# Optimization experiments

Hardware: AMD Instinct MI355X
Metric: run time of the kernel (lower is better)

## Reference

```python
import jax, jax.numpy as jnp
import numpy as np

B, H, NCAND = 2048, 1024, 4  # batch, hidden_size, l candidates


def setup_inputs() -> dict:
    key = jax.random.key(0)
    ks = jax.random.split(key, 5)
    s = 1.0 / np.sqrt(H)  # torch uniform(-1/sqrt(H), 1/sqrt(H)) init
    L = jax.random.uniform(ks[0], (NCAND, H, H), minval=-s, maxval=s, dtype=jnp.float32)
    R = jax.random.uniform(ks[1], (NCAND, H, H), minval=-s, maxval=s, dtype=jnp.float32)
    # candidate 3 is initialized to identity in the original module
    L = L.at[3].set(jnp.eye(H, dtype=jnp.float32))
    R = R.at[3].set(jnp.eye(H, dtype=jnp.float32))
    b = jnp.zeros((NCAND, H), dtype=jnp.float32)
    w_score = jax.random.uniform(ks[2], (H,), minval=-s, maxval=s, dtype=jnp.float32)
    x = jax.random.normal(ks[3], (B, 1, H), dtype=jnp.float32)
    h_prev = jax.random.normal(ks[4], (B, 1, H), dtype=jnp.float32)
    return {"x": x, "h_prev": h_prev, "L": L, "R": R, "b": b, "w_score": w_score}


def _mix(lst, w_score):
    # lst: [B, 4, H] candidate vectors; score each candidate, softmax-combine.
    scores = jnp.einsum('bkh,h->bk', lst, w_score)          # [B, 4]
    probs = jax.nn.softmax(scores, axis=-1)
    out = jnp.einsum('bk,bkh->bh', probs, lst)              # [B, H]
    return out, jnp.argmax(scores, axis=-1)


def _lin(v, W):
    # v: [B, H], W: [4, H, H] -> all 4 candidate transforms: [B, 4, H]
    return jnp.einsum('bh,khd->bkd', v, W)


def reference(x, h_prev, L, R, b, w_score):
    xs = x[:, 0, :]        # [B, H]
    hs = h_prev[:, 0, :]   # [B, H]
    bb = b[None]           # [1, 4, H]

    z1 = jax.nn.sigmoid(xs @ L[0] + hs @ R[0] + b[0])
    r = jax.nn.sigmoid(xs @ L[1] + hs @ R[1] + b[1])
    z2 = jax.nn.sigmoid(xs @ L[0] + hs @ R[0] + b[0])  # identical expression to z1, as in source

    # stage 3: rh = mix_k( (h@Lk) * (r@Rk) + bk )
    rh, g3 = _mix(_lin(hs, L) * _lin(r, R) + bb, w_score)
    # stage 4: h_tilde = mix_k( tanh(x@Lk + rh@Rk + bk) )
    h_tilde, g4 = _mix(jnp.tanh(_lin(xs, L) + _lin(rh, R) + bb), w_score)
    # stage 5: 1 - (z1@Rk + bk)
    one_minus_z1, g5 = _mix(1.0 - (_lin(z1, R) + bb), w_score)
    # stage 6: (h_tilde@Lk) * (one_minus_z1@Rk) + bk
    zh_tilde, g6 = _mix(_lin(h_tilde, L) * _lin(one_minus_z1, R) + bb, w_score)
    # stage 7: (h@Lk) * (z2@Rk) + bk
    z2h, g7 = _mix(_lin(hs, L) * _lin(z2, R) + bb, w_score)
    # stage 8: zh_tilde@Lk + z2h@Rk + bk
    h_next, g8 = _mix(_lin(zh_tilde, L) + _lin(z2h, R) + bb, w_score)

    G = jnp.zeros((x.shape[0], 9), dtype=jnp.int32)
    G = (G.at[:, 3].set(g3).at[:, 4].set(g4).at[:, 5].set(g5)
          .at[:, 6].set(g6).at[:, 7].set(g7).at[:, 8].set(g8))
    return h_next[:, None, :], G
```

## Files before the change

### kernel.cpp

```cpp
#include <hip/hip_runtime.h>
#include <math.h>

#define B 2048
#define H 1024
#define HH (1024 * 1024)

typedef __attribute__((ext_vector_type(8))) short bf16x8;
typedef __attribute__((ext_vector_type(4))) float floatx4;

__device__ __forceinline__ short bf16_rne(float x) {
    unsigned int b = __float_as_uint(x);
    unsigned int r = (b + 0x7fffu + ((b >> 16) & 1u)) >> 16;
    return (short)r;
}
__device__ __forceinline__ float bf16_f(short h) {
    return __uint_as_float(((unsigned int)(unsigned short)h) << 16);
}
__device__ __forceinline__ void split2(float x, short& h, short& l) {
    h = bf16_rne(x);
    l = bf16_rne(x - bf16_f(h));
}
__device__ __forceinline__ float ld3(const float* f, const short* h, const short* l, size_t i) {
    if (f) return f[i];
    return bf16_f(h[i]) + bf16_f(l[i]);
}

__device__ __forceinline__ void gl16(const void* g, void* l) {
    __builtin_amdgcn_global_load_lds(
        (const __attribute__((address_space(1))) void*)g,
        (__attribute__((address_space(3))) void*)l, 16, 0, 0);
}

struct Job {
    const short* ah; const short* al;
    const short* wh; const short* wl;
    float* c;
    long ldc;
};
struct Jobs { Job j[8]; };

__global__ __launch_bounds__(256, 2) void gemm_kernel(Jobs jobs)
{
    __shared__ short lds[2][4][4096];
    const int bid = blockIdx.x;
    const int z = bid >> 7;
    const int mi = (bid & 127) >> 3, ni = bid & 7;
    const Job jb = jobs.j[z];
    const int tid = threadIdx.x;
    const int w = tid >> 6, lane = tid & 63;
    const int wm = w >> 1, wn = w & 1;
    const int m0 = mi * 128, n0 = ni * 128;

    const int cid0 = tid, cid1 = 256 + tid;
    const int r0 = cid0 >> 2, g0 = (((cid0 & 3) ^ ((cid0 >> 3) & 3)) << 3);
    const int r1 = cid1 >> 2, g1 = (((cid1 & 3) ^ ((cid1 >> 3) & 3)) << 3);

    const short* p0[4] = { jb.ah + (size_t)(m0 + r0) * H + g0,
                           jb.al + (size_t)(m0 + r0) * H + g0,
                           jb.wh + (size_t)(n0 + r0) * H + g0,
                           jb.wl + (size_t)(n0 + r0) * H + g0 };
    const short* p1[4] = { jb.ah + (size_t)(m0 + r1) * H + g1,
                           jb.al + (size_t)(m0 + r1) * H + g1,
                           jb.wh + (size_t)(n0 + r1) * H + g1,
                           jb.wl + (size_t)(n0 + r1) * H + g1 };

    const int fr = lane & 15, kc = lane >> 4;
    int aoff[4], boff[4];
#pragma unroll
    for (int t = 0; t < 4; t++) {
        int ar = wm * 64 + t * 16 + fr;
        aoff[t] = ar * 32 + ((kc ^ ((ar >> 1) & 3)) << 3);
        int br = wn * 64 + t * 16 + fr;
        boff[t] = br * 32 + ((kc ^ ((br >> 1) & 3)) << 3);
    }

    floatx4 acc[4][4];
#pragma unroll
    for (int i = 0; i < 4; i++)
#pragma unroll
        for (int j = 0; j < 4; j++) acc[i][j] = (floatx4)0.f;

#define ISSUE8(P)                                                        \
    do {                                                                 \
        _Pragma("unroll")                                                \
        for (int o = 0; o < 4; o++) {                                    \
            gl16(p0[o], &lds[P][o][w * 512]);                            \
            gl16(p1[o], &lds[P][o][2048 + w * 512]);                     \
            p0[o] += 32; p1[o] += 32;                                    \
        }                                                                \
    } while (0)

#define COMPUTE(P)                                                       \
    do {                                                                 \
        bf16x8 fah[4], fal[4], fbh[4], fbl[4];                           \
        _Pragma("unroll")                                                \
        for (int t = 0; t < 4; t++) {                                    \
            fah[t] = *(const bf16x8*)&lds[P][0][aoff[t]];                \
            fal[t] = *(const bf16x8*)&lds[P][1][aoff[t]];                \
            fbh[t] = *(const bf16x8*)&lds[P][2][boff[t]];                \
            fbl[t] = *(const bf16x8*)&lds[P][3][boff[t]];                \
        }                                                                \
        _Pragma("unroll")                                                \
        for (int mt = 0; mt < 4; mt++)                                   \
            _Pragma("unroll")                                            \
            for (int nt = 0; nt < 4; nt++) {                             \
                acc[mt][nt] = __builtin_amdgcn_mfma_f32_16x16x32_bf16(fah[mt], fbh[nt], acc[mt][nt], 0, 0, 0); \
                acc[mt][nt] = __builtin_amdgcn_mfma_f32_16x16x32_bf16(fah[mt], fbl[nt], acc[mt][nt], 0, 0, 0); \
                acc[mt][nt] = __builtin_amdgcn_mfma_f32_16x16x32_bf16(fal[mt], fbh[nt], acc[mt][nt], 0, 0, 0); \
                acc[mt][nt] = __builtin_amdgcn_mfma_f32_16x16x32_bf16(fal[mt], fbl[nt], acc[mt][nt], 0, 0, 0); \
            }                                                            \
    } while (0)

    ISSUE8(0);
    for (int ks = 0; ks < 32; ks += 2) {
        __syncthreads();
        ISSUE8(1);
        COMPUTE(0);
        __syncthreads();
        if (ks + 2 < 32) ISSUE8(0);
        COMPUTE(1);
    }
#undef ISSUE8
#undef COMPUTE

    const int cr = (lane >> 4) * 4, cc = lane & 15;
#pragma unroll
    for (int mt = 0; mt < 4; mt++)
#pragma unroll
        for (int nt = 0; nt < 4; nt++) {
            float* Cp = jb.c + (size_t)(m0 + wm * 64 + mt * 16 + cr) * jb.ldc
                             + n0 + wn * 64 + nt * 16 + cc;
#pragma unroll
            for (int i = 0; i < 4; i++) Cp[(size_t)i * jb.ldc] = acc[mt][nt][i];
        }
}

__global__ __launch_bounds__(256) void wsplit_kernel(
    const float* __restrict__ L, const float* __restrict__ R,
    short* __restrict__ Lth, short* __restrict__ Ltl,
    short* __restrict__ Rth, short* __restrict__ Rtl)
{
    const int zz = blockIdx.z;
    const float* W = (zz < 3) ? L : R;
    short* Oh = (zz < 3) ? Lth : Rth;
    short* Ol = (zz < 3) ? Ltl : Rtl;
    const int z = (zz < 3) ? zz : zz - 3;
    const int k0 = blockIdx.y * 32, n0 = blockIdx.x * 32;
    __shared__ float t[32][33];
    const int tx = threadIdx.x & 31, ty = threadIdx.x >> 5;
    const float* src = W + (size_t)z * HH;
#pragma unroll
    for (int j = 0; j < 4; j++) {
        int r = ty + j * 8;
        t[r][tx] = src[(size_t)(k0 + r) * 1024 + n0 + tx];
    }
    __syncthreads();
    short* oh = Oh + (size_t)z * HH;
    short* ol = Ol + (size_t)z * HH;
#pragma unroll
    for (int j = 0; j < 4; j++) {
        int n = ty + j * 8;
        float v = t[tx][n];
        short hh, ll; split2(v, hh, ll);
        oh[(size_t)(n0 + n) * 1024 + k0 + tx] = hh;
        ol[(size_t)(n0 + n) * 1024 + k0 + tx] = ll;
    }
}

__global__ __launch_bounds__(256) void conv_kernel(
    const float* __restrict__ xs, const float* __restrict__ hs,
    short* __restrict__ xh, short* __restrict__ xl,
    short* __restrict__ hh, short* __restrict__ hl)
{
    size_t i = (size_t)blockIdx.x * 256 + threadIdx.x;
    short a, b2; split2(xs[i], a, b2); xh[i] = a; xl[i] = b2;
    split2(hs[i], a, b2); hh[i] = a; hl[i] = b2;
}

__global__ __launch_bounds__(256) void zero_g_kernel(float* __restrict__ G)
{
    int idx = blockIdx.x * 256 + threadIdx.x;
    if (idx < B * 9) G[idx] = 0.f;
}

__global__ __launch_bounds__(256) void e0_kernel(
    const float* __restrict__ xsL, const float* __restrict__ hsR,
    const float* __restrict__ bias,
    short* __restrict__ z1h, short* __restrict__ z1l,
    short* __restrict__ rh_, short* __restrict__ rl_)
{
    size_t idx = (size_t)blockIdx.x * 256 + threadIdx.x;
    int b = (int)(idx >> 10), h = (int)(idx & 1023);
    float z1 = 1.f / (1.f + expf(-(xsL[(size_t)b * 3072 + h] + hsR[(size_t)b * 2048 + h] + bias[h])));
    float r  = 1.f / (1.f + expf(-(xsL[(size_t)b * 3072 + 1024 + h] + hsR[(size_t)b * 2048 + 1024 + h] + bias[1024 + h])));
    short hh, ll;
    split2(z1, hh, ll); z1h[idx] = hh; z1l[idx] = ll;
    split2(r, hh, ll);  rh_[idx] = hh; rl_[idx] = ll;
}

__device__ __forceinline__ float wave_red(float v)
{
#pragma unroll
    for (int o = 32; o; o >>= 1) v += __shfl_down(v, o, 64);
    return v;
}

__global__ __launch_bounds__(256) void mix2_kernel(
    const float* __restrict__ hsL, const float* __restrict__ z1R,
    const short* __restrict__ z1h_, const short* __restrict__ z1l_,
    const float* __restrict__ hsf,
    const float* __restrict__ bias, const float* __restrict__ wsc,
    short* __restrict__ omzh, short* __restrict__ omzl,
    short* __restrict__ z2hh, short* __restrict__ z2hl,
    float* __restrict__ G)
{
    const int b = blockIdx.x, tid = threadIdx.x;
    const size_t base = (size_t)b * 3072;
    const size_t vbase = (size_t)b * 1024;
    float v[2][4][4], sc[2][4];
#pragma unroll
    for (int m = 0; m < 2; m++)
#pragma unroll
        for (int k = 0; k < 4; k++) sc[m][k] = 0.f;
#pragma unroll
    for (int k = 0; k < 4; k++)
#pragma unroll
        for (int i = 0; i < 4; i++) {
            int h = tid + i * 256;
            float hl, zr;
            if (k < 3) {
                hl = hsL[base + k * 1024 + h];
                zr = z1R[base + k * 1024 + h];
            } else {
                hl = hsf[vbase + h];
                zr = bf16_f(z1h_[vbase + h]) + bf16_f(z1l_[vbase + h]);
            }
            float bk = bias[k * 1024 + h];
            float wv = wsc[h];
            float c = 1.0f - (zr + bk);
            float d = fmaf(hl, zr, bk);
            v[0][k][i] = c; v[1][k][i] = d;
            sc[0][k] = fmaf(c, wv, sc[0][k]);
            sc[1][k] = fmaf(d, wv, sc[1][k]);
        }
    __shared__ float red[8][4];
    const int wid = tid >> 6, lane = tid & 63;
#pragma unroll
    for (int m = 0; m < 2; m++)
#pragma unroll
        for (int k = 0; k < 4; k++) {
            float s = wave_red(sc[m][k]);
            if (lane == 0) red[m * 4 + k][wid] = s;
        }
    __syncthreads();
    __shared__ float probs[2][4];
    if (tid < 2) {
        int m = tid;
        float s[4];
#pragma unroll
        for (int k = 0; k < 4; k++)
            s[k] = red[m * 4 + k][0] + red[m * 4 + k][1] + red[m * 4 + k][2] + red[m * 4 + k][3];
        int am = 0; float mx = s[0];
#pragma unroll
        for (int k = 1; k < 4; k++) if (s[k] > mx) { mx = s[k]; am = k; }
        float e[4], tot = 0.f;
#pragma unroll
        for (int k = 0; k < 4; k++) { e[k] = expf(s[k] - mx); tot += e[k]; }
#pragma unroll
        for (int k = 0; k < 4; k++) probs[m][k] = e[k] / tot;
        G[(size_t)b * 9 + (m == 0 ? 5 : 7)] = (float)am;
    }
    __syncthreads();
    float p0[4], p1[4];
#pragma unroll
    for (int k = 0; k < 4; k++) { p0[k] = probs[0][k]; p1[k] = probs[1][k]; }
#pragma unroll
    for (int i = 0; i < 4; i++) {
        int h = tid + i * 256;
        float o0 = 0, o1 = 0;
#pragma unroll
        for (int k = 0; k < 4; k++) {
            o0 = fmaf(p0[k], v[0][k][i], o0);
            o1 = fmaf(p1[k], v[1][k][i], o1);
        }
        short hh, ll;
        split2(o0, hh, ll); omzh[vbase + h] = hh; omzl[vbase + h] = ll;
        split2(o1, hh, ll); z2hh[vbase + h] = hh; z2hl[vbase + h] = ll;
    }
}

template <int OP>
__global__ __launch_bounds__(256) void mix_kernel(
    const float* __restrict__ P, const float* __restrict__ Q,
    const float* __restrict__ a3f, const short* __restrict__ a3h, const short* __restrict__ a3l,
    const float* __restrict__ b3f, const short* __restrict__ b3h, const short* __restrict__ b3l,
    const float* __restrict__ bias, const float* __restrict__ wsc,
    float* __restrict__ of, short* __restrict__ oh, short* __restrict__ ol,
    float* __restrict__ G, int gcol)
{
    const int b = blockIdx.x, tid = threadIdx.x;
    const size_t base = (size_t)b * 3072;
    const size_t vbase = (size_t)b * 1024;
    float v[4][4];
    float sc[4] = {0.f, 0.f, 0.f, 0.f};
#pragma unroll
    for (int k = 0; k < 4; k++)
#pragma unroll
        for (int i = 0; i < 4; i++) {
            int h = tid + i * 256;
            float pp, qq;
            if (k < 3) {
                pp = P[base + k * 1024 + h];
                qq = Q[base + k * 1024 + h];
            } else {
                pp = ld3(a3f, a3h, a3l, vbase + h);
                qq = ld3(b3f, b3h, b3l, vbase + h);
            }
            float bk = bias[k * 1024 + h];
            float val;
            if (OP == 0)      val = fmaf(pp, qq, bk);
            else if (OP == 1) val = tanhf(pp + qq + bk);
            else              val = pp + qq + bk;
            v[k][i] = val;
            sc[k] = fmaf(val, wsc[h], sc[k]);
        }
    __shared__ float red[4][4];
    const int wid = tid >> 6, lane = tid & 63;
#pragma unroll
    for (int k = 0; k < 4; k++) {
        float s = wave_red(sc[k]);
        if (lane == 0) red[k][wid] = s;
    }
    __syncthreads();
    __shared__ float probs[4];
    if (tid == 0) {
        float s[4];
#pragma unroll
        for (int k = 0; k < 4; k++)
            s[k] = red[k][0] + red[k][1] + red[k][2] + red[k][3];
        int am = 0; float mx = s[0];
#pragma unroll
        for (int k = 1; k < 4; k++) if (s[k] > mx) { mx = s[k]; am = k; }
        float e[4], tot = 0.f;
#pragma unroll
        for (int k = 0; k < 4; k++) { e[k] = expf(s[k] - mx); tot += e[k]; }
#pragma unroll
        for (int k = 0; k < 4; k++) probs[k] = e[k] / tot;
        G[(size_t)b * 9 + gcol] = (float)am;
    }
    __syncthreads();
    float p0 = probs[0], p1 = probs[1], p2 = probs[2], p3 = probs[3];
#pragma unroll
    for (int i = 0; i < 4; i++) {
        int h = tid + i * 256;
        float o = p0 * v[0][i];
        o = fmaf(p1, v[1][i], o);
        o = fmaf(p2, v[2][i], o);
        o = fmaf(p3, v[3][i], o);
        if (oh) {
            short hh, ll; split2(o, hh, ll);
            oh[vbase + h] = hh;
            ol[vbase + h] = ll;
        } else {
            of[vbase + h] = o;
        }
    }
}

extern "C" void kernel_launch(void* const* d_in, const int* in_sizes, int n_in,
                              void* d_out, int out_size, void* d_ws, size_t ws_size,
                              hipStream_t stream)
{
    const float* xs   = (const float*)d_in[0];
    const float* hs   = (const float*)d_in[1];
    const float* L    = (const float*)d_in[2];
    const float* R    = (const float*)d_in[3];
    const float* bias = (const float*)d_in[4];
    const float* w    = (const float*)d_in[5];

    float* out = (float*)d_out;
    float* G   = out + (size_t)B * H;

    char* wsb = (char*)d_ws;
    const size_t MB = 1024ull * 1024;
    float* fA = (float*)(wsb);
    float* fB = (float*)(wsb + 24 * MB);
    float* fC = (float*)(wsb + 48 * MB);
    float* fD = (float*)(wsb + 72 * MB);
    short* P1h = (short*)(wsb + 96 * MB);  short* P1l = P1h + 2 * MB;
    short* P2h = (short*)(wsb + 104 * MB); short* P2l = P2h + 2 * MB;
    short* P3h = (short*)(wsb + 112 * MB); short* P3l = P3h + 2 * MB;
    short* P4h = (short*)(wsb + 120 * MB); short* P4l = P4h + 2 * MB;
    short* Lth = (short*)(wsb + 128 * MB);
    short* Ltl = (short*)(wsb + 134 * MB);
    short* Rth = (short*)(wsb + 140 * MB);
    short* Rtl = (short*)(wsb + 146 * MB);

    dim3 blk(256);
    const float* NF = nullptr; const short* NS = nullptr;

    conv_kernel<<<(B * H) / 256, blk, 0, stream>>>(xs, hs, P1h, P1l, P2h, P2l);
    wsplit_kernel<<<dim3(32, 32, 6), blk, 0, stream>>>(L, R, Lth, Ltl, Rth, Rtl);
    zero_g_kernel<<<(B * 9 + 255) / 256, blk, 0, stream>>>(G);

    Jobs s0{};
    for (int p = 0; p < 3; p++) {
        s0.j[p]     = { P1h, P1l, Lth + (size_t)p * HH, Ltl + (size_t)p * HH, fA + p * 1024, 3072 };
        s0.j[3 + p] = { P2h, P2l, Lth + (size_t)p * HH, Ltl + (size_t)p * HH, fB + p * 1024, 3072 };
    }
    for (int p = 0; p < 2; p++)
        s0.j[6 + p] = { P2h, P2l, Rth + (size_t)p * HH, Rtl + (size_t)p * HH, fC + p * 1024, 2048 };
    gemm_kernel<<<dim3(8 * 128), blk, 0, stream>>>(s0);

    e0_kernel<<<(B * H) / 256, blk, 0, stream>>>(fA, fC, bias, P3h, P3l, P4h, P4l);

    Jobs s1{};
    for (int p = 0; p < 3; p++) {
        s1.j[p]     = { P3h, P3l, Rth + (size_t)p * HH, Rtl + (size_t)p * HH, fD + p * 1024, 3072 };
        s1.j[3 + p] = { P4h, P4l, Rth + (size_t)p * HH, Rtl + (size_t)p * HH, fC + p * 1024, 3072 };
    }
    gemm_kernel<<<dim3(6 * 128), blk, 0, stream>>>(s1);

    mix2_kernel<<<B, blk, 0, stream>>>(fB, fD, P3h, P3l, hs, bias, w,
                                       P2h, P2l, P3h, P3l, G);
    mix_kernel<0><<<B, blk, 0, stream>>>(fB, fC, hs, NS, NS, NF, P4h, P4l,
                                         bias, w, nullptr, P1h, P1l, G, 3);

    Jobs s2{};
    for (int p = 0; p < 3; p++) {
        s2.j[p]     = { P1h, P1l, Rth + (size_t)p * HH, Rtl + (size_t)p * HH, fB + p * 1024, 3072 };
        s2.j[3 + p] = { P2h, P2l, Rth + (size_t)p * HH, Rtl + (size_t)p * HH, fC + p * 1024, 3072 };
    }
    gemm_kernel<<<dim3(6 * 128), blk, 0, stream>>>(s2);

    mix_kernel<1><<<B, blk, 0, stream>>>(fA, fB, xs, NS, NS, NF, P1h, P1l,
                                         bias, w, nullptr, P4h, P4l, G, 4);

    Jobs s3{};
    for (int p = 0; p < 3; p++) {
        s3.j[p]     = { P4h, P4l, Lth + (size_t)p * HH, Ltl + (size_t)p * HH, fA + p * 1024, 3072 };
        s3.j[3 + p] = { P3h, P3l, Rth + (size_t)p * HH, Rtl + (size_t)p * HH, fB + p * 1024, 3072 };
    }
    gemm_kernel<<<dim3(6 * 128), blk, 0, stream>>>(s3);

    mix_kernel<0><<<B, blk, 0, stream>>>(fA, fC, NF, P4h, P4l, NF, P2h, P2l,
                                         bias, w, nullptr, P1h, P1l, G, 6);

    Jobs s4{};
    for (int p = 0; p < 3; p++)
        s4.j[p] = { P1h, P1l, Lth + (size_t)p * HH, Ltl + (size_t)p * HH, fC + p * 1024, 3072 };
    gemm_kernel<<<dim3(3 * 128), blk, 0, stream>>>(s4);

    mix_kernel<2><<<B, blk, 0, stream>>>(fC, fB, NF, P1h, P1l, NF, P3h, P3l,
                                         bias, w, out, nullptr, nullptr, G, 8);
}
```

Measured before the change: 608.6 us.

## Remap GEMM block indices for XCD-aware locality and split the first grouped GEMM

Changes the blockIdx-to-(job, m-tile, n-tile) mapping so that blocks landing on the same XCD (bid & 7) share a group of jobs and n-tiles. Same-XCD blocks then reuse weight and activation tiles in their local L2. The first 8-job GEMM launch is split into two launches grouped by shared A operand (5 jobs on P2, 3 jobs on P1). The split adds a kernel launch, and the uneven job grouping could hurt load balance.

```diff
diff --git a/kernel.cpp b/kernel.cpp
--- a/kernel.cpp
+++ b/kernel.cpp
@@ -39,12 +39,21 @@
 };
 struct Jobs { Job j[8]; };
 
-__global__ __launch_bounds__(256, 2) void gemm_kernel(Jobs jobs)
+__global__ __launch_bounds__(256, 2) void gemm_kernel(Jobs jobs, int gs, int zpg)
 {
     __shared__ short lds[2][4][4096];
     const int bid = blockIdx.x;
-    const int z = bid >> 7;
-    const int mi = (bid & 127) >> 3, ni = bid & 7;
+    const int x = bid & 7;
+    const int s = bid >> 3;
+    const int g = x >> gs;
+    const int xl = x & ((1 << gs) - 1);
+    const int niPer = 8 >> gs;
+    const int inner = zpg * niPer;
+    const int mi = s / inner;
+    const int r = s - mi * inner;
+    const int z = g * zpg + r / niPer;
+    const int ni = xl * niPer + (r - (r / niPer) * niPer);
+
     const Job jb = jobs.j[z];
     const int tid = threadIdx.x;
     const int w = tid >> 6, lane = tid & 63;
@@ -403,14 +412,17 @@
     wsplit_kernel<<<dim3(32, 32, 6), blk, 0, stream>>>(L, R, Lth, Ltl, Rth, Rtl);
     zero_g_kernel<<<(B * 9 + 255) / 256, blk, 0, stream>>>(G);
 
-    Jobs s0{};
-    for (int p = 0; p < 3; p++) {
-        s0.j[p]     = { P1h, P1l, Lth + (size_t)p * HH, Ltl + (size_t)p * HH, fA + p * 1024, 3072 };
-        s0.j[3 + p] = { P2h, P2l, Lth + (size_t)p * HH, Ltl + (size_t)p * HH, fB + p * 1024, 3072 };
-    }
+    Jobs d1{};
+    for (int p = 0; p < 3; p++)
+        d1.j[p] = { P2h, P2l, Lth + (size_t)p * HH, Ltl + (size_t)p * HH, fB + p * 1024, 3072 };
     for (int p = 0; p < 2; p++)
-        s0.j[6 + p] = { P2h, P2l, Rth + (size_t)p * HH, Rtl + (size_t)p * HH, fC + p * 1024, 2048 };
-    gemm_kernel<<<dim3(8 * 128), blk, 0, stream>>>(s0);
+        d1.j[3 + p] = { P2h, P2l, Rth + (size_t)p * HH, Rtl + (size_t)p * HH, fC + p * 1024, 2048 };
+    gemm_kernel<<<dim3(128 * 5), blk, 0, stream>>>(d1, 3, 5);
+
+    Jobs d2{};
+    for (int p = 0; p < 3; p++)
+        d2.j[p] = { P1h, P1l, Lth + (size_t)p * HH, Ltl + (size_t)p * HH, fA + p * 1024, 3072 };
+    gemm_kernel<<<dim3(128 * 3), blk, 0, stream>>>(d2, 3, 3);
 
     e0_kernel<<<(B * H) / 256, blk, 0, stream>>>(fA, fC, bias, P3h, P3l, P4h, P4l);
 
@@ -419,7 +431,7 @@
         s1.j[p]     = { P3h, P3l, Rth + (size_t)p * HH, Rtl + (size_t)p * HH, fD + p * 1024, 3072 };
         s1.j[3 + p] = { P4h, P4l, Rth + (size_t)p * HH, Rtl + (size_t)p * HH, fC + p * 1024, 3072 };
     }
-    gemm_kernel<<<dim3(6 * 128), blk, 0, stream>>>(s1);
+    gemm_kernel<<<dim3(128 * 6), blk, 0, stream>>>(s1, 2, 3);
 
     mix2_kernel<<<B, blk, 0, stream>>>(fB, fD, P3h, P3l, hs, bias, w,
                                        P2h, P2l, P3h, P3l, G);
@@ -431,7 +443,7 @@
         s2.j[p]     = { P1h, P1l, Rth + (size_t)p * HH, Rtl + (size_t)p * HH, fB + p * 1024, 3072 };
         s2.j[3 + p] = { P2h, P2l, Rth + (size_t)p * HH, Rtl + (size_t)p * HH, fC + p * 1024, 3072 };
     }
-    gemm_kernel<<<dim3(6 * 128), blk, 0, stream>>>(s2);
+    gemm_kernel<<<dim3(128 * 6), blk, 0, stream>>>(s2, 2, 3);
 
     mix_kernel<1><<<B, blk, 0, stream>>>(fA, fB, xs, NS, NS, NF, P1h, P1l,
                                          bias, w, nullptr, P4h, P4l, G, 4);
@@ -441,7 +453,7 @@
         s3.j[p]     = { P4h, P4l, Lth + (size_t)p * HH, Ltl + (size_t)p * HH, fA + p * 1024, 3072 };
         s3.j[3 + p] = { P3h, P3l, Rth + (size_t)p * HH, Rtl + (size_t)p * HH, fB + p * 1024, 3072 };
     }
-    gemm_kernel<<<dim3(6 * 128), blk, 0, stream>>>(s3);
+    gemm_kernel<<<dim3(128 * 6), blk, 0, stream>>>(s3, 2, 3);
 
     mix_kernel<0><<<B, blk, 0, stream>>>(fA, fC, NF, P4h, P4l, NF, P2h, P2l,
                                          bias, w, nullptr, P1h, P1l, G, 6);
@@ -449,7 +461,7 @@
     Jobs s4{};
     for (int p = 0; p < 3; p++)
         s4.j[p] = { P1h, P1l, Lth + (size_t)p * HH, Ltl + (size_t)p * HH, fC + p * 1024, 3072 };
-    gemm_kernel<<<dim3(3 * 128), blk, 0, stream>>>(s4);
+    gemm_kernel<<<dim3(128 * 3), blk, 0, stream>>>(s4, 3, 3);
 
     mix_kernel<2><<<B, blk, 0, stream>>>(fC, fB, NF, P1h, P1l, NF, P3h, P3l,
                                          bias, w, out, nullptr, nullptr, G, 8);
```

Result: no change. 612.2 us (+0.6%).
